# Optimization experiments

Hardware: AMD Instinct MI355X
Metric: run time of the kernel (lower is better)

Reference implementation:

```python
import jax, jax.numpy as jnp
import numpy as np

N_GRAPHS = 5000
NODES_PER_GRAPH = 100
EDGES_PER_GRAPH = 400
N_NODES = N_GRAPHS * NODES_PER_GRAPH
N_EDGES = N_GRAPHS * EDGES_PER_GRAPH
K = 2
DIMS = [74, 70, 65, 60, 55, 37]


def setup_inputs() -> dict:
    key = jax.random.key(0)
    ks = jax.random.split(key, 16)
    x = jax.random.normal(ks[0], (N_NODES, DIMS[0]), dtype=jnp.float32)
    # edges constrained within each graph: base node offset per graph + random local node
    edge_base = (jnp.arange(N_EDGES, dtype=jnp.int32) // EDGES_PER_GRAPH) * NODES_PER_GRAPH
    src = edge_base + jax.random.randint(ks[1], (N_EDGES,), 0, NODES_PER_GRAPH, dtype=jnp.int32)
    dst = edge_base + jax.random.randint(ks[2], (N_EDGES,), 0, NODES_PER_GRAPH, dtype=jnp.int32)
    graph_ids = (jnp.arange(N_NODES, dtype=jnp.int32) // NODES_PER_GRAPH)
    inp = {"x": x, "src": src, "dst": dst, "graph_ids": graph_ids}
    # TAGConv weights: Linear(in*(K+1) -> out) + bias, for each of 5 layers
    for i in range(5):
        fan_in = DIMS[i] * (K + 1)
        w = jax.random.normal(ks[3 + 2 * i], (fan_in, DIMS[i + 1]), dtype=jnp.float32) / np.sqrt(fan_in)
        b = jnp.zeros((DIMS[i + 1],), dtype=jnp.float32)
        inp[f"W{i}"] = w
        inp[f"b{i}"] = b
    inp["gate_w"] = jax.random.normal(ks[13], (DIMS[-1], 1), dtype=jnp.float32) / np.sqrt(DIMS[-1])
    inp["gate_b"] = jnp.zeros((1,), dtype=jnp.float32)
    return inp


def _forward(x, src, dst, graph_ids, Ws, bs, gate_w, gate_b):
    n = x.shape[0]
    # symmetric normalization with in-degree (DGL TAGConv convention), clamp min 1
    deg = jax.ops.segment_sum(jnp.ones_like(src, dtype=x.dtype), dst, num_segments=n)
    norm = jnp.clip(deg, 1.0, None) ** -0.5  # [N]
    norm = norm[:, None]

    def tagconv(h, W, b):
        feats = [h]
        cur = h
        for _ in range(K):
            msg = (cur * norm)[src]  # gather over edges
            cur = norm * jax.ops.segment_sum(msg, dst, num_segments=n)
            feats.append(cur)
        return jnp.concatenate(feats, axis=-1) @ W + b

    h = x
    for W, b in zip(Ws, bs):
        h = jax.nn.relu(tagconv(h, W, b))

    # GlobalAttentionPooling: per-graph softmax over gate scores, weighted sum
    gate = (h @ gate_w + gate_b)[:, 0]  # [N]
    gmax = jax.ops.segment_max(gate, graph_ids, num_segments=N_GRAPHS)
    e = jnp.exp(gate - gmax[graph_ids])
    z = jax.ops.segment_sum(e, graph_ids, num_segments=N_GRAPHS)
    alpha = e / z[graph_ids]
    pooled = jax.ops.segment_sum(h * alpha[:, None], graph_ids, num_segments=N_GRAPHS)  # [G, 37]
    return pooled.reshape(-1, 2, DIMS[-1])


def reference(x, src, dst, graph_ids, W0, b0, W1, b1, W2, b2, W3, b3, W4, b4, gate_w, gate_b):
    Ws = [W0, W1, W2, W3, W4]
    bs = [b0, b1, b2, b3, b4]
    return _forward(x, src, dst, graph_ids, Ws, bs, gate_w, gate_b)
```

## Files before the change

### kernel.cpp

```cpp
#include <hip/hip_runtime.h>
#include <math.h>


typedef __attribute__((ext_vector_type(8))) short bf16x8;
typedef __attribute__((ext_vector_type(4))) float f32x4;

constexpr int NODES  = 100;
constexpr int EDGES  = 400;
constexpr int STRIDE = 76;
constexpr int NTHR   = 512;

__device__ __align__(16) unsigned g_packW[86016];

struct __align__(16) Smem {
    float bufA[NODES * STRIDE];
    float bufB[NODES * STRIDE];
    float csr_val[EDGES];
    unsigned short csr_src[EDGES];
    int   row_start[NODES + 1];
    int   cntg[NODES];
    float nrm[NODES];
};

union FragU { unsigned u[4]; uint4 q; bf16x8 s; };

__device__ __forceinline__ void split_pair(float a, float b,
                                           unsigned& h, unsigned& l) {
    unsigned ua = __float_as_uint(a), ub = __float_as_uint(b);
    unsigned ha = ua & 0xFFFF0000u,  hb = ub & 0xFFFF0000u;
    h = (ua >> 16) | hb;
    float ra = a - __uint_as_float(ha);
    float rb = b - __uint_as_float(hb);
    l = (__float_as_uint(ra) >> 16) | (__float_as_uint(rb) & 0xFFFF0000u);
}

template<int D_IN, int D_OUT, int KT, int NT, int WOFF_U32>
__device__ __forceinline__ void repack_layer(const float* __restrict__ W, int idx) {
    constexpr int TILES = 3 * KT * NT;
    if (idx >= TILES * 64) return;
    int lane = idx & 63, tile = idx >> 6;
    int nt = tile % NT;
    int kt = (tile / NT) % KT;
    int b  = tile / (NT * KT);
    int col = nt * 16 + (lane & 15);
    int kg  = (lane >> 4) << 2;
    float v[8];
#pragma unroll
    for (int i = 0; i < 8; ++i) {
        int k = kt * 32 + ((i >= 4) ? 16 : 0) + kg + (i & 3);
        float f = 0.f;
        if (k < D_IN && col < D_OUT) f = W[(b * D_IN + k) * D_OUT + col];
        v[i] = f;
    }
    unsigned hu[4], lu[4];
#pragma unroll
    for (int p = 0; p < 4; ++p) split_pair(v[2*p], v[2*p+1], hu[p], lu[p]);
    unsigned* dst = g_packW + WOFF_U32 + (tile * 64 + lane) * 8;
    *(uint4*)(dst)     = make_uint4(hu[0], hu[1], hu[2], hu[3]);
    *(uint4*)(dst + 4) = make_uint4(lu[0], lu[1], lu[2], lu[3]);
}

__global__ void repack_kernel(const float* __restrict__ W0, const float* __restrict__ W1,
                              const float* __restrict__ W2, const float* __restrict__ W3,
                              const float* __restrict__ W4) {
    int idx = blockIdx.x * 256 + threadIdx.x;
    switch (blockIdx.y) {
    case 0: repack_layer<74, 70, 3, 5,     0>(W0, idx); break;
    case 1: repack_layer<70, 65, 3, 5, 23040>(W1, idx); break;
    case 2: repack_layer<65, 60, 3, 4, 46080>(W2, idx); break;
    case 3: repack_layer<60, 55, 2, 4, 64512>(W3, idx); break;
    case 4: repack_layer<55, 37, 2, 3, 76800>(W4, idx); break;
    }
}

template<int D_IN>
__device__ __forceinline__ void propagate(const float* __restrict__ in,
                                          float* __restrict__ outb,
                                          const unsigned short* __restrict__ csr_src,
                                          const float* __restrict__ csr_val,
                                          const int* __restrict__ row_start,
                                          const float* __restrict__ nrm,
                                          int wave, int lane)
{
    constexpr int CH = (D_IN + 3) / 4;
    constexpr int PR = (CH + 1) / 2;
    constexpr int T  = NODES * PR;
    constexpr int R4 = STRIDE / 4;
    const float4* __restrict__ in4 = (const float4*)in;
    float4* __restrict__ out4 = (float4*)outb;

    const int lo = (T * (6 * wave)) / 56;
    const int hi = (wave == 7) ? T : (T * (6 * (wave + 1))) / 56;

    for (int t = lo + lane; t < hi; t += 64) {
        int n = t / PR;
        int p = t - n * PR;
        int c0 = 2 * p;
        int c1 = c0 + 1;
        bool has2 = (c1 < CH);
        int c1r = has2 ? c1 : c0;
        int beg = row_start[n], end = row_start[n + 1];
        float ax0 = 0.f, ay0 = 0.f, az0 = 0.f, aw0 = 0.f;
        float ax1 = 0.f, ay1 = 0.f, az1 = 0.f, aw1 = 0.f;
        int e = beg;
        for (; e + 3 < end; e += 4) {
            int   s0 = csr_src[e],     s1 = csr_src[e + 1];
            int   s2 = csr_src[e + 2], s3 = csr_src[e + 3];
            float q0 = csr_val[e],     q1 = csr_val[e + 1];
            float q2 = csr_val[e + 2], q3 = csr_val[e + 3];
            const float4* r0 = in4 + s0 * R4;
            const float4* r1 = in4 + s1 * R4;
            const float4* r2 = in4 + s2 * R4;
            const float4* r3 = in4 + s3 * R4;
            float4 u0 = r0[c0], v0 = r0[c1r];
            float4 u1 = r1[c0], v1 = r1[c1r];
            float4 u2 = r2[c0], v2 = r2[c1r];
            float4 u3 = r3[c0], v3 = r3[c1r];
            ax0 = fmaf(q0, u0.x, ax0); ay0 = fmaf(q0, u0.y, ay0);
            az0 = fmaf(q0, u0.z, az0); aw0 = fmaf(q0, u0.w, aw0);
            ax1 = fmaf(q0, v0.x, ax1); ay1 = fmaf(q0, v0.y, ay1);
            az1 = fmaf(q0, v0.z, az1); aw1 = fmaf(q0, v0.w, aw1);
            ax0 = fmaf(q1, u1.x, ax0); ay0 = fmaf(q1, u1.y, ay0);
            az0 = fmaf(q1, u1.z, az0); aw0 = fmaf(q1, u1.w, aw0);
            ax1 = fmaf(q1, v1.x, ax1); ay1 = fmaf(q1, v1.y, ay1);
            az1 = fmaf(q1, v1.z, az1); aw1 = fmaf(q1, v1.w, aw1);
            ax0 = fmaf(q2, u2.x, ax0); ay0 = fmaf(q2, u2.y, ay0);
            az0 = fmaf(q2, u2.z, az0); aw0 = fmaf(q2, u2.w, aw0);
            ax1 = fmaf(q2, v2.x, ax1); ay1 = fmaf(q2, v2.y, ay1);
            az1 = fmaf(q2, v2.z, az1); aw1 = fmaf(q2, v2.w, aw1);
            ax0 = fmaf(q3, u3.x, ax0); ay0 = fmaf(q3, u3.y, ay0);
            az0 = fmaf(q3, u3.z, az0); aw0 = fmaf(q3, u3.w, aw0);
            ax1 = fmaf(q3, v3.x, ax1); ay1 = fmaf(q3, v3.y, ay1);
            az1 = fmaf(q3, v3.z, az1); aw1 = fmaf(q3, v3.w, aw1);
        }
        for (; e < end; ++e) {
            int s = csr_src[e];
            float q = csr_val[e];
            const float4* r = in4 + s * R4;
            float4 u = r[c0], v = r[c1r];
            ax0 = fmaf(q, u.x, ax0); ay0 = fmaf(q, u.y, ay0);
            az0 = fmaf(q, u.z, az0); aw0 = fmaf(q, u.w, aw0);
            ax1 = fmaf(q, v.x, ax1); ay1 = fmaf(q, v.y, ay1);
            az1 = fmaf(q, v.z, az1); aw1 = fmaf(q, v.w, aw1);
        }
        float sn = nrm[n];
        float4 o0 = { ax0 * sn, ay0 * sn, az0 * sn, aw0 * sn };
        out4[n * R4 + c0] = o0;
        if (has2) {
            float4 o1 = { ax1 * sn, ay1 * sn, az1 * sn, aw1 * sn };
            out4[n * R4 + c1] = o1;
        }
    }
}

template<int D_IN, int D_OUT, int KT, int NT, int WOFF_U32>
__device__ __forceinline__ void dense_block(const float* __restrict__ buf, int b,
                                            int mt, int lane, f32x4 (&acc)[NT]) {
    int row = mt * 16 + (lane & 15);
    row = row > NODES - 1 ? NODES - 1 : row;
    const float* __restrict__ hrow = buf + row * STRIDE;
    const int kg = (lane >> 4) << 2;
    const uint4* __restrict__ wb =
        (const uint4*)(g_packW + WOFF_U32) + b * (KT * NT * 128) + lane * 2;
#pragma unroll
    for (int kt = 0; kt < KT; ++kt) {
        int o0 = kt * 32 + kg;      if (o0 > 72) o0 = 72;
        int o1 = kt * 32 + 16 + kg; if (o1 > 72) o1 = 72;
        const float4 f0 = *(const float4*)(hrow + o0);
        const float4 f1 = *(const float4*)(hrow + o1);
        FragU Ah, Al;
        split_pair(f0.x, f0.y, Ah.u[0], Al.u[0]);
        split_pair(f0.z, f0.w, Ah.u[1], Al.u[1]);
        split_pair(f1.x, f1.y, Ah.u[2], Al.u[2]);
        split_pair(f1.z, f1.w, Ah.u[3], Al.u[3]);
#pragma unroll
        for (int nt = 0; nt < NT; ++nt) {
            const uint4* __restrict__ wl = wb + (kt * NT + nt) * 128;
            FragU Bh, Bl;
            Bh.q = wl[0];
            Bl.q = wl[1];
            acc[nt] = __builtin_amdgcn_mfma_f32_16x16x32_bf16(Ah.s, Bh.s, acc[nt], 0, 0, 0);
            acc[nt] = __builtin_amdgcn_mfma_f32_16x16x32_bf16(Ah.s, Bl.s, acc[nt], 0, 0, 0);
            acc[nt] = __builtin_amdgcn_mfma_f32_16x16x32_bf16(Al.s, Bh.s, acc[nt], 0, 0, 0);
        }
    }
}

template<int D_IN, int D_OUT, int KT, int NT, int WOFF_U32>
__device__ __forceinline__ void tag_layer(Smem& sm,
                                          float* __restrict__ S,
                                          float* __restrict__ T,
                                          const float* __restrict__ Bv,
                                          int tid)
{
    const int wave  = __builtin_amdgcn_readfirstlane(tid >> 6);
    const int lane  = tid & 63;
    const bool m_act = wave < 7;

    f32x4 acc[NT];
#pragma unroll
    for (int nt = 0; nt < NT; ++nt) acc[nt] = (f32x4)(0.f);

    if (m_act) dense_block<D_IN, D_OUT, KT, NT, WOFF_U32>(S, 0, wave, lane, acc);
    propagate<D_IN>(S, T, sm.csr_src, sm.csr_val, sm.row_start, sm.nrm, wave, lane);
    __syncthreads();
    if (m_act) dense_block<D_IN, D_OUT, KT, NT, WOFF_U32>(T, 1, wave, lane, acc);
    propagate<D_IN>(T, S, sm.csr_src, sm.csr_val, sm.row_start, sm.nrm, wave, lane);
    __syncthreads();
    if (m_act) {
        dense_block<D_IN, D_OUT, KT, NT, WOFF_U32>(S, 2, wave, lane, acc);
#pragma unroll
        for (int nt = 0; nt < NT; ++nt) {
            int col = nt * 16 + (lane & 15);
            if (col < D_OUT) {
                float bias = Bv[col];
#pragma unroll
                for (int r = 0; r < 4; ++r) {
                    int row = wave * 16 + ((lane >> 4) << 2) + r;
                    if (row < NODES)
                        T[row * STRIDE + col] = fmaxf(acc[nt][r] + bias, 0.f);
                }
            }
        }
    }
    __syncthreads();
}

__global__ __launch_bounds__(NTHR, 2)
void drug_graph_conv_kernel(
    const float* __restrict__ x,
    const int*   __restrict__ src,
    const int*   __restrict__ dst,
    const float* __restrict__ b0, const float* __restrict__ b1,
    const float* __restrict__ b2, const float* __restrict__ b3,
    const float* __restrict__ b4,
    const float* __restrict__ gate_w, const float* __restrict__ gate_b,
    float* __restrict__ out)
{
    __shared__ Smem sm;
    const int g     = blockIdx.x;
    const int tid   = threadIdx.x;
    const int nbase = g * NODES;

    {
        const float4* __restrict__ x4 = (const float4*)(x + (size_t)nbase * 74);
        for (int t = tid; t < NODES * 74 / 4; t += NTHR) {
            float4 v = x4[t];
            int idx = 4 * t;
#pragma unroll
            for (int k = 0; k < 4; ++k) {
                int ik = idx + k;
                int n  = ik / 74;
                int d  = ik - n * 74;
                float val = (k == 0) ? v.x : (k == 1) ? v.y : (k == 2) ? v.z : v.w;
                sm.bufA[n * STRIDE + d] = val;
            }
        }
    }
    for (int t = tid; t < NODES * 2; t += NTHR) {
        int n = t >> 1;
        sm.bufA[n * STRIDE + 74 + (t & 1)] = 0.f;
    }

    if (tid < NODES) sm.cntg[tid] = 0;
    __syncthreads();
    int es = 0, ed = 0;
    const bool ethr = tid < EDGES;
    if (ethr) {
        es = src[g * EDGES + tid] - nbase;
        ed = dst[g * EDGES + tid] - nbase;
        atomicAdd(&sm.cntg[ed], 1);
    }
    __syncthreads();

    if (tid < NODES) sm.nrm[tid] = rsqrtf((float)max(sm.cntg[tid], 1));
    if (tid < 64) {
        int v1 = (tid < NODES) ? sm.cntg[tid] : 0;
        int l2 = tid + 64;
        int v2 = (l2 < NODES) ? sm.cntg[l2] : 0;
        int s1 = v1;
#pragma unroll
        for (int d = 1; d < 64; d <<= 1) {
            int t2 = __shfl_up(s1, d, 64);
            if (tid >= d) s1 += t2;
        }
        int tot1 = __shfl(s1, 63, 64);
        int s2 = v2;
#pragma unroll
        for (int d = 1; d < 64; d <<= 1) {
            int t2 = __shfl_up(s2, d, 64);
            if (tid >= d) s2 += t2;
        }
        s2 += tot1;
        if (tid == 0) sm.row_start[0] = 0;
        sm.row_start[tid + 1] = s1;
        if (l2 < NODES) sm.row_start[l2 + 1] = s2;
    }
    __syncthreads();
    if (tid < NODES) sm.cntg[tid] = 0;
    __syncthreads();
    if (ethr) {
        int pos = atomicAdd(&sm.cntg[ed], 1);
        int slot = sm.row_start[ed] + pos;
        sm.csr_src[slot] = (unsigned short)es;
        sm.csr_val[slot] = sm.nrm[es];
    }
    __syncthreads();

    tag_layer<74, 70, 3, 5,     0>(sm, sm.bufA, sm.bufB, b0, tid);
    tag_layer<70, 65, 3, 5, 23040>(sm, sm.bufB, sm.bufA, b1, tid);
    tag_layer<65, 60, 3, 4, 46080>(sm, sm.bufA, sm.bufB, b2, tid);
    tag_layer<60, 55, 2, 4, 64512>(sm, sm.bufB, sm.bufA, b3, tid);
    tag_layer<55, 37, 2, 3, 76800>(sm, sm.bufA, sm.bufB, b4, tid);

    float* gate = (float*)sm.cntg;
    if (tid < NODES) {
        float s = gate_b[0];
#pragma unroll
        for (int k = 0; k < 37; ++k)
            s = fmaf(sm.bufB[tid * STRIDE + k], gate_w[k], s);
        gate[tid] = s;
    }
    __syncthreads();
    if (tid < 64) {
        float v1 = (tid < NODES) ? gate[tid] : -INFINITY;
        float v2 = (tid + 64 < NODES) ? gate[tid + 64] : -INFINITY;
        float m = fmaxf(v1, v2);
#pragma unroll
        for (int d = 32; d; d >>= 1) m = fmaxf(m, __shfl_xor(m, d, 64));
        float e1 = (tid < NODES) ? __expf(v1 - m) : 0.f;
        float e2 = (tid + 64 < NODES) ? __expf(v2 - m) : 0.f;
        float z = e1 + e2;
#pragma unroll
        for (int d = 32; d; d >>= 1) z += __shfl_xor(z, d, 64);
        float inv = 1.f / z;
        if (tid < NODES) gate[tid] = e1 * inv;
        if (tid + 64 < NODES) gate[tid + 64] = e2 * inv;
    }
    __syncthreads();

    {
        const int w = tid >> 6, l = tid & 63;
        if (l < 37) {
            float p = 0.f;
            for (int n = w; n < NODES; n += 8)
                p = fmaf(gate[n], sm.bufB[n * STRIDE + l], p);
            sm.csr_val[w * 37 + l] = p;
        }
    }
    __syncthreads();
    if (tid < 37) {
        float p = 0.f;
#pragma unroll
        for (int w = 0; w < 8; ++w) p += sm.csr_val[w * 37 + tid];
        out[g * 37 + tid] = p;
    }
}

extern "C" void kernel_launch(void* const* d_in, const int* in_sizes, int n_in,
                              void* d_out, int out_size, void* d_ws, size_t ws_size,
                              hipStream_t stream) {
    const float* x   = (const float*)d_in[0];
    const int*   src = (const int*)  d_in[1];
    const int*   dst = (const int*)  d_in[2];
    const float* W0 = (const float*)d_in[4];  const float* b0 = (const float*)d_in[5];
    const float* W1 = (const float*)d_in[6];  const float* b1 = (const float*)d_in[7];
    const float* W2 = (const float*)d_in[8];  const float* b2 = (const float*)d_in[9];
    const float* W3 = (const float*)d_in[10]; const float* b3 = (const float*)d_in[11];
    const float* W4 = (const float*)d_in[12]; const float* b4 = (const float*)d_in[13];
    const float* gw = (const float*)d_in[14]; const float* gb = (const float*)d_in[15];
    float* out = (float*)d_out;

    dim3 rg(12, 5, 1);
    repack_kernel<<<rg, 256, 0, stream>>>(W0, W1, W2, W3, W4);

    drug_graph_conv_kernel<<<5000, NTHR, 0, stream>>>(
        x, src, dst, b0, b1, b2, b3, b4, gw, gb, out);
}
```

Baseline: 807.6 us.

## Sort nodes by in-degree and interleave propagate work blocks across waves

```diff
diff --git a/kernel.cpp b/kernel.cpp
--- a/kernel.cpp
+++ b/kernel.cpp
@@ -20,6 +20,8 @@
     int   row_start[NODES + 1];
     int   cntg[NODES];
     float nrm[NODES];
+    int   hist[64];
+    unsigned short order[NODES];
 };
 
 union FragU { unsigned u[4]; uint4 q; bf16x8 s; };
@@ -80,23 +82,25 @@
                                           const float* __restrict__ csr_val,
                                           const int* __restrict__ row_start,
                                           const float* __restrict__ nrm,
+                                          const unsigned short* __restrict__ order,
                                           int wave, int lane)
 {
     constexpr int CH = (D_IN + 3) / 4;
     constexpr int PR = (CH + 1) / 2;
     constexpr int T  = NODES * PR;
+    constexpr int NB = (T + 63) / 64;
     constexpr int R4 = STRIDE / 4;
     const float4* __restrict__ in4 = (const float4*)in;
     float4* __restrict__ out4 = (float4*)outb;
 
-    const int lo = (T * (6 * wave)) / 56;
-    const int hi = (wave == 7) ? T : (T * (6 * (wave + 1))) / 56;
-
-    for (int t = lo + lane; t < hi; t += 64) {
-        int n = t / PR;
-        int p = t - n * PR;
-        int c0 = 2 * p;
-        int c1 = c0 + 1;
+    auto do_block = [&](int j) {
+        int t = (j << 6) + lane;
+        if (t >= T) return;
+        int r = t / PR;
+        int p = t - r * PR;
+        int n = order[r];
+        int c0 = p;
+        int c1 = p + PR;
         bool has2 = (c1 < CH);
         int c1r = has2 ? c1 : c0;
         int beg = row_start[n], end = row_start[n + 1];
@@ -136,8 +140,8 @@
         for (; e < end; ++e) {
             int s = csr_src[e];
             float q = csr_val[e];
-            const float4* r = in4 + s * R4;
-            float4 u = r[c0], v = r[c1r];
+            const float4* rr = in4 + s * R4;
+            float4 u = rr[c0], v = rr[c1r];
             ax0 = fmaf(q, u.x, ax0); ay0 = fmaf(q, u.y, ay0);
             az0 = fmaf(q, u.z, az0); aw0 = fmaf(q, u.w, aw0);
             ax1 = fmaf(q, v.x, ax1); ay1 = fmaf(q, v.y, ay1);
@@ -150,6 +154,13 @@
             float4 o1 = { ax1 * sn, ay1 * sn, az1 * sn, aw1 * sn };
             out4[n * R4 + c1] = o1;
         }
+    };
+
+    if (wave < 7) {
+        for (int j = wave; j < NB; j += 9) do_block(j);
+    } else {
+        for (int j = 7; j < NB; j += 9) do_block(j);
+        for (int j = 8; j < NB; j += 9) do_block(j);
     }
 }
 
@@ -202,10 +213,12 @@
     for (int nt = 0; nt < NT; ++nt) acc[nt] = (f32x4)(0.f);
 
     if (m_act) dense_block<D_IN, D_OUT, KT, NT, WOFF_U32>(S, 0, wave, lane, acc);
-    propagate<D_IN>(S, T, sm.csr_src, sm.csr_val, sm.row_start, sm.nrm, wave, lane);
+    propagate<D_IN>(S, T, sm.csr_src, sm.csr_val, sm.row_start, sm.nrm,
+                    sm.order, wave, lane);
     __syncthreads();
     if (m_act) dense_block<D_IN, D_OUT, KT, NT, WOFF_U32>(T, 1, wave, lane, acc);
-    propagate<D_IN>(T, S, sm.csr_src, sm.csr_val, sm.row_start, sm.nrm, wave, lane);
+    propagate<D_IN>(T, S, sm.csr_src, sm.csr_val, sm.row_start, sm.nrm,
+                    sm.order, wave, lane);
     __syncthreads();
     if (m_act) {
         dense_block<D_IN, D_OUT, KT, NT, WOFF_U32>(S, 2, wave, lane, acc);
@@ -274,6 +287,7 @@
     __syncthreads();
 
     if (tid < NODES) sm.nrm[tid] = rsqrtf((float)max(sm.cntg[tid], 1));
+    if (tid >= 128 && tid < 192) sm.hist[tid - 128] = 0;
     if (tid < 64) {
         int v1 = (tid < NODES) ? sm.cntg[tid] : 0;
         int l2 = tid + 64;
@@ -297,6 +311,26 @@
         if (l2 < NODES) sm.row_start[l2 + 1] = s2;
     }
     __syncthreads();
+
+    if (tid < NODES) atomicAdd(&sm.hist[min(sm.cntg[tid], 63)], 1);
+    __syncthreads();
+    if (tid < 64) {
+        int v = sm.hist[tid];
+        int s = v;
+#pragma unroll
+        for (int d = 1; d < 64; d <<= 1) {
+            int t2 = __shfl_up(s, d, 64);
+            if (tid >= d) s += t2;
+        }
+        sm.hist[tid] = s - v;
+    }
+    __syncthreads();
+    if (tid < NODES) {
+        int pos = atomicAdd(&sm.hist[min(sm.cntg[tid], 63)], 1);
+        sm.order[pos] = (unsigned short)tid;
+    }
+    __syncthreads();
+
     if (tid < NODES) sm.cntg[tid] = 0;
     __syncthreads();
     if (ethr) {
```

Result: faster. 771.1 us (-4.5%).
